# Performance work log

Hardware: AMD Instinct MI355X
Metric: run time of the kernel (lower is better)

Reference implementation:

```python
import jax, jax.numpy as jnp
import numpy as np

B, N, F, H = 2, 2048, 1024, 16
D = F // H  # head_dim = 64
SCALE = D ** -0.5


def setup_inputs() -> dict:
    key = jax.random.key(0)
    ks = jax.random.split(key, 5)
    std = F ** -0.5
    return {
        "x": jax.random.normal(ks[0], (B, N, F), dtype=jnp.float32),
        "Wq": jax.random.normal(ks[1], (F, F), dtype=jnp.float32) * std,
        "Wk": jax.random.normal(ks[2], (F, F), dtype=jnp.float32) * std,
        "Wv": jax.random.normal(ks[3], (F, F), dtype=jnp.float32) * std,
        "Wo": jax.random.normal(ks[4], (F, F), dtype=jnp.float32) * std,
        "bo": jnp.zeros((F,), dtype=jnp.float32),
    }


def reference(x, Wq, Wk, Wv, Wo, bo):
    b, n, f = x.shape
    # nn.Linear computes x @ W.T
    q = (x @ Wq.T).reshape(b, n, H, D).transpose(0, 2, 1, 3)  # bhnd
    k = (x @ Wk.T).reshape(b, n, H, D).transpose(0, 2, 1, 3)
    v = (x @ Wv.T).reshape(b, n, H, D).transpose(0, 2, 1, 3)
    score = jax.nn.softmax(jnp.einsum('bhif,bhjf->bhij', q, k) * SCALE, axis=-1)
    attn = jnp.einsum('bhij,bhjf->bihf', score, v)  # (b, n, h, d)
    o = attn.reshape(b, n, f) @ Wo.T + bo
    return o
```

## Files before the change

### kernel.cpp

```cpp
#include <hip/hip_runtime.h>
#include <hip/hip_bf16.h>

#define B_    2
#define NSEQ  2048
#define FDIM  1024
#define NH    16
#define HD    64
#define MTOT  (B_*NSEQ)
#define BHSZ  (NSEQ*HD)

typedef __bf16 bf16_t;
typedef __bf16 bf16x4 __attribute__((ext_vector_type(4)));
typedef __bf16 bf16x8 __attribute__((ext_vector_type(8)));
typedef float  f32x4  __attribute__((ext_vector_type(4)));

#define AS1 __attribute__((address_space(1)))
#define AS3 __attribute__((address_space(3)))

__device__ __forceinline__ void gld_lds16(const bf16_t* g, bf16_t* l) {
  __builtin_amdgcn_global_load_lds((const AS1 void*)g, (AS3 void*)l, 16, 0, 0);
}

__device__ __forceinline__ f32x4 mfma_pv(bf16x4 a, bf16x4 b, f32x4 c) {
#if defined(__HIP_DEVICE_COMPILE__)
#if __has_builtin(__builtin_amdgcn_mfma_f32_16x16x16bf16_1k)
  typedef short s4 __attribute__((ext_vector_type(4)));
  return __builtin_amdgcn_mfma_f32_16x16x16bf16_1k(
      __builtin_bit_cast(s4, a), __builtin_bit_cast(s4, b), c, 0, 0, 0);
#else
  asm("v_mfma_f32_16x16x16_bf16 %0, %1, %2, %0" : "+v"(c) : "v"(a), "v"(b));
  return c;
#endif
#else
  (void)a; (void)b;
  return c;
#endif
}

__device__ __forceinline__ float fexp2(float x) {
#if defined(__HIP_DEVICE_COMPILE__)
#if __has_builtin(__builtin_amdgcn_exp2f)
  return __builtin_amdgcn_exp2f(x);
#else
  return exp2f(x);
#endif
#else
  return exp2f(x);
#endif
}

extern "C" __global__ __launch_bounds__(256) void cast_all_k(
    const float* __restrict__ x,  const float* __restrict__ wq,
    const float* __restrict__ wk, const float* __restrict__ wv,
    const float* __restrict__ wo,
    bf16_t* __restrict__ xb,  bf16_t* __restrict__ wqb,
    bf16_t* __restrict__ wkb, bf16_t* __restrict__ wvb,
    bf16_t* __restrict__ wob)
{
  long t = (long)blockIdx.x * blockDim.x + threadIdx.x;
  long i = t * 4;
  const float* src; bf16_t* dst; long off;
  if      (i < 4194304L) { src = x;  dst = xb;  off = i; }
  else if (i < 5242880L) { src = wq; dst = wqb; off = i - 4194304L; }
  else if (i < 6291456L) { src = wk; dst = wkb; off = i - 5242880L; }
  else if (i < 7340032L) { src = wv; dst = wvb; off = i - 6291456L; }
  else                   { src = wo; dst = wob; off = i - 7340032L; }
  float4 v = *(const float4*)(src + off);
  bf16x4 o = { (bf16_t)v.x, (bf16_t)v.y, (bf16_t)v.z, (bf16_t)v.w };
  *(bf16x4*)(dst + off) = o;
}

extern "C" __global__ __launch_bounds__(256) void gemm_bt_k(
    const bf16_t* __restrict__ A,
    const bf16_t* __restrict__ Bq, const bf16_t* __restrict__ Bk,
    const bf16_t* __restrict__ Bv,
    bf16_t* __restrict__ oq, bf16_t* __restrict__ okk,
    bf16_t* __restrict__ ovt, float* __restrict__ oo,
    const float* __restrict__ bias, int mode_base)
{
  __shared__ __align__(16) bf16_t As[2*128*32];
  __shared__ __align__(16) bf16_t Bs[2*128*32];
  const int K = FDIM;
  int mode = mode_base + blockIdx.z;
  const bf16_t* Bw = (mode == 0) ? Bq : (mode == 1) ? Bk : (mode == 2) ? Bv : Bq;
  int m0 = blockIdx.y * 128, n0 = blockIdx.x * 128;
  int tid = threadIdx.x, lane = tid & 63, wave = tid >> 6;
  int g = lane >> 4, c = lane & 15;
  int wm = (wave >> 1) * 64, wn = (wave & 1) * 64;
  f32x4 acc[4][4];
  for (int i = 0; i < 4; ++i)
    for (int j = 0; j < 4; ++j)
      acc[i][j] = (f32x4){0.f, 0.f, 0.f, 0.f};

  int srow = lane >> 2;
  int scol = (lane & 3) * 8;

  for (int kt = 0; kt < K / 64; ++kt) {
    int kk = kt * 64;
    for (int cc = 0; cc < 2; ++cc) {
      int chunk = wave * 2 + cc;
      const bf16_t* ag = A  + (long)(m0 + chunk*16 + srow) * K + kk + scol;
      const bf16_t* bg = Bw + (long)(n0 + chunk*16 + srow) * K + kk + scol;
      gld_lds16(ag,      As + chunk * 512);
      gld_lds16(ag + 32, As + 4096 + chunk * 512);
      gld_lds16(bg,      Bs + chunk * 512);
      gld_lds16(bg + 32, Bs + 4096 + chunk * 512);
    }
    __syncthreads();
    bf16x8 af[4][2], bfr[4][2];
    for (int t = 0; t < 4; ++t) {
      af[t][0]  = *(const bf16x8*)(As + (wm + t*16 + c) * 32 + g * 8);
      af[t][1]  = *(const bf16x8*)(As + 4096 + (wm + t*16 + c) * 32 + g * 8);
      bfr[t][0] = *(const bf16x8*)(Bs + (wn + t*16 + c) * 32 + g * 8);
      bfr[t][1] = *(const bf16x8*)(Bs + 4096 + (wn + t*16 + c) * 32 + g * 8);
    }
    for (int mt = 0; mt < 4; ++mt)
      for (int nt = 0; nt < 4; ++nt) {
        acc[mt][nt] = __builtin_amdgcn_mfma_f32_16x16x32_bf16(
            af[mt][0], bfr[nt][0], acc[mt][nt], 0, 0, 0);
        acc[mt][nt] = __builtin_amdgcn_mfma_f32_16x16x32_bf16(
            af[mt][1], bfr[nt][1], acc[mt][nt], 0, 0, 0);
      }
    __syncthreads();
  }

  if (mode == 0) {
    const float QSC = 0.125f * 1.44269504088896340736f;
    for (int mt = 0; mt < 4; ++mt)
      for (int nt = 0; nt < 4; ++nt) {
        int n = n0 + wn + nt*16 + c;
        int h = n >> 6, d = n & 63;
        for (int r = 0; r < 4; ++r) {
          int m = m0 + wm + mt*16 + g*4 + r;
          int b = m >> 11, tok = m & 2047;
          oq[((long)(b*NH + h) * NSEQ + tok) * HD + d] =
              (bf16_t)(acc[mt][nt][r] * QSC);
        }
      }
  } else if (mode == 1) {
    for (int mt = 0; mt < 4; ++mt)
      for (int nt = 0; nt < 4; ++nt) {
        int n = n0 + wn + nt*16 + c;
        int h = n >> 6, d = n & 63;
        int kh = d >> 5, gK = (d >> 3) & 3, e = d & 7;
        for (int r = 0; r < 4; ++r) {
          int m = m0 + wm + mt*16 + g*4 + r;
          int b = m >> 11, tok = m & 2047;
          int tile = tok >> 6, mtA = (tok >> 4) & 3, cA = tok & 15;
          okk[(long)(b*NH + h) * BHSZ + tile*4096
              + (mtA*2 + kh)*512 + (gK*16 + cA)*8 + e] = (bf16_t)acc[mt][nt][r];
        }
      }
  } else if (mode == 2) {
    for (int mt = 0; mt < 4; ++mt)
      for (int nt = 0; nt < 4; ++nt) {
        int n = n0 + wn + nt*16 + c;
        int h = n >> 6, d = n & 63;
        int dtA = d >> 4, cA = d & 15;
        int m = m0 + wm + mt*16 + g*4;
        int b = m >> 11, tok = m & 2047;
        int tile = tok >> 6, mtA = (tok >> 4) & 3, gA = (tok >> 2) & 3;
        bf16x4 pk = { (bf16_t)acc[mt][nt][0], (bf16_t)acc[mt][nt][1],
                      (bf16_t)acc[mt][nt][2], (bf16_t)acc[mt][nt][3] };
        *(bf16x4*)(ovt + (long)(b*NH + h) * BHSZ + tile*4096
                   + (mtA*4 + dtA)*256 + (cA*4 + gA)*4) = pk;
      }
  } else {
    for (int mt = 0; mt < 4; ++mt)
      for (int nt = 0; nt < 4; ++nt) {
        int n = n0 + wn + nt*16 + c;
        float bv = bias[n];
        for (int r = 0; r < 4; ++r) {
          int m = m0 + wm + mt*16 + g*4 + r;
          oo[(long)m * FDIM + n] = acc[mt][nt][r] + bv;
        }
      }
  }
}

extern "C" __global__ __launch_bounds__(512) void attn_fused_k(
    const bf16_t* __restrict__ q, const bf16_t* __restrict__ k,
    const bf16_t* __restrict__ vt, bf16_t* __restrict__ attn)
{
  __shared__ __align__(16) char arena[65536];
  __shared__ float Ll[128];
  int bh = blockIdx.y;
  int tid = threadIdx.x, lane = tid & 63, wave = tid >> 6;
  int g = lane >> 4, c = lane & 15;
  int qg = wave & 3, half = wave >> 2;
  int qw = blockIdx.x * 128 + qg * 32;
  const bf16_t* Q  = q  + (long)bh * NSEQ * HD;
  const bf16_t* Kf = k  + (long)bh * BHSZ;
  const bf16_t* Vf = vt + (long)bh * BHSZ;

  bf16x8 bQ[2][2];
#pragma unroll
  for (int s = 0; s < 2; ++s)
#pragma unroll
    for (int hh = 0; hh < 2; ++hh)
      bQ[s][hh] = *(const bf16x8*)(Q + (long)(qw + s*16 + c) * HD + hh*32 + g*8);

  f32x4 acc[2][4];
  f32x4 lsum[2];
#pragma unroll
  for (int s = 0; s < 2; ++s) {
#pragma unroll
    for (int dt = 0; dt < 4; ++dt) acc[s][dt] = (f32x4){0.f, 0.f, 0.f, 0.f};
    lsum[s] = (f32x4){0.f, 0.f, 0.f, 0.f};
  }

  int w4 = wave & 3, ln = lane;
  const int NT = NSEQ / 128;
  int kbase = half * (NSEQ / 2);

  auto stage = [&](int buf, int k0) {
    bf16_t* Kb = (bf16_t*)(arena + buf * 32768 + half * 16384);
    bf16_t* Vb = Kb + 4096;
    long tbase = (long)(k0 >> 6) * 4096;
#pragma unroll
    for (int j = 0; j < 2; ++j) {
      int ch = j*4 + w4;
      gld_lds16(Kf + tbase + ch*512 + ln*8, Kb + ch*512);
      gld_lds16(Vf + tbase + ch*512 + ln*8, Vb + ch*512);
    }
  };

  stage(0, kbase);
  __syncthreads();

  for (int kt = 0; kt < NT; ++kt) {
    int cur = kt & 1;
    if (kt + 1 < NT) stage(cur ^ 1, kbase + (kt + 1) * 64);

    const bf16_t* Kb = (const bf16_t*)(arena + cur * 32768 + half * 16384);
    const bf16_t* Vb = Kb + 4096;

    f32x4 St[2][4];
#pragma unroll
    for (int mt = 0; mt < 4; ++mt) {
      bf16x8 k0f = *(const bf16x8*)(Kb + (mt*2 + 0) * 512 + lane * 8);
      bf16x8 k1f = *(const bf16x8*)(Kb + (mt*2 + 1) * 512 + lane * 8);
#pragma unroll
      for (int s = 0; s < 2; ++s) {
        f32x4 z = (f32x4){0.f, 0.f, 0.f, 0.f};
        z = __builtin_amdgcn_mfma_f32_16x16x32_bf16(k0f, bQ[s][0], z, 0, 0, 0);
        z = __builtin_amdgcn_mfma_f32_16x16x32_bf16(k1f, bQ[s][1], z, 0, 0, 0);
        St[s][mt] = z;
      }
    }

    bf16x4 bP[2][4];
#pragma unroll
    for (int s = 0; s < 2; ++s)
#pragma unroll
      for (int mt = 0; mt < 4; ++mt) {
#pragma unroll
        for (int r = 0; r < 4; ++r) {
          float p = fexp2(St[s][mt][r]);
          St[s][mt][r] = p;
          lsum[s][r] += p;
        }
        bP[s][mt] = (bf16x4){(bf16_t)St[s][mt][0], (bf16_t)St[s][mt][1],
                             (bf16_t)St[s][mt][2], (bf16_t)St[s][mt][3]};
      }

#pragma unroll
    for (int mt = 0; mt < 4; ++mt)
#pragma unroll
      for (int dt = 0; dt < 4; ++dt) {
        bf16x4 aV = *(const bf16x4*)(Vb + (mt*4 + dt) * 256 + (c*4 + g) * 4);
        acc[0][dt] = mfma_pv(aV, bP[0][mt], acc[0][dt]);
        acc[1][dt] = mfma_pv(aV, bP[1][mt], acc[1][dt]);
      }

    __syncthreads();
  }

  float lp[2];
#pragma unroll
  for (int s = 0; s < 2; ++s) {
    float p = (lsum[s][0] + lsum[s][1]) + (lsum[s][2] + lsum[s][3]);
    p += __shfl_xor(p, 16);
    p += __shfl_xor(p, 32);
    lp[s] = p;
  }

  float* Opart = (float*)arena;
  bf16_t* Tb = (bf16_t*)(arena + 36864);
  if (half == 1) {
#pragma unroll
    for (int s = 0; s < 2; ++s) {
      int qrow = qg*32 + s*16 + c;
#pragma unroll
      for (int dt = 0; dt < 4; ++dt)
        *(f32x4*)(Opart + qrow*72 + dt*16 + g*4) = acc[s][dt];
      if (g == 0) Ll[qrow] = lp[s];
    }
  }
  __syncthreads();
  if (half == 0) {
#pragma unroll
    for (int s = 0; s < 2; ++s) {
      int qrow = qg*32 + s*16 + c;
      float inv = 1.f / (lp[s] + Ll[qrow]);
#pragma unroll
      for (int dt = 0; dt < 4; ++dt) {
        f32x4 part = *(const f32x4*)(Opart + qrow*72 + dt*16 + g*4);
#pragma unroll
        for (int r = 0; r < 4; ++r)
          Tb[qrow*80 + dt*16 + g*4 + r] =
              (bf16_t)((acc[s][dt][r] + part[r]) * inv);
      }
    }
  }
  __syncthreads();
  int b = bh >> 4, h = bh & 15;
  int row = tid >> 2, dseg = (tid & 3) * 16;
  const bf16_t* src = Tb + row*80 + dseg;
  bf16_t* dst = attn + ((long)(b * NSEQ + blockIdx.x*128 + row)) * FDIM + h * HD + dseg;
  *(bf16x8*)(dst)     = *(const bf16x8*)(src);
  *(bf16x8*)(dst + 8) = *(const bf16x8*)(src + 8);
}

extern "C" void kernel_launch(void* const* d_in, const int* in_sizes, int n_in,
                              void* d_out, int out_size, void* d_ws, size_t ws_size,
                              hipStream_t stream)
{
  const float* x  = (const float*)d_in[0];
  const float* wq = (const float*)d_in[1];
  const float* wk = (const float*)d_in[2];
  const float* wv = (const float*)d_in[3];
  const float* wo = (const float*)d_in[4];
  const float* bo = (const float*)d_in[5];
  float* out = (float*)d_out;
  char* ws = (char*)d_ws;

  const size_t MB = 1024 * 1024;
  bf16_t* xb    = (bf16_t*)(ws);
  bf16_t* wqb   = (bf16_t*)(ws + 8  * MB);
  bf16_t* wkb   = (bf16_t*)(ws + 10 * MB);
  bf16_t* wvb   = (bf16_t*)(ws + 12 * MB);
  bf16_t* wob   = (bf16_t*)(ws + 14 * MB);
  bf16_t* q_ws  = (bf16_t*)(ws + 16 * MB);
  bf16_t* k_ws  = (bf16_t*)(ws + 24 * MB);
  bf16_t* vt_ws = (bf16_t*)(ws + 32 * MB);
  bf16_t* at_ws = (bf16_t*)(ws + 40 * MB);

  hipLaunchKernelGGL(cast_all_k, dim3(8192), dim3(256), 0, stream,
                     x, wq, wk, wv, wo, xb, wqb, wkb, wvb, wob);

  hipLaunchKernelGGL(gemm_bt_k, dim3(8, 32, 3), dim3(256), 0, stream,
                     xb, wqb, wkb, wvb, q_ws, k_ws, vt_ws,
                     (float*)nullptr, (const float*)nullptr, 0);

  hipLaunchKernelGGL(attn_fused_k, dim3(16, 32), dim3(512), 0, stream,
                     q_ws, k_ws, vt_ws, at_ws);

  hipLaunchKernelGGL(gemm_bt_k, dim3(8, 32, 1), dim3(256), 0, stream,
                     at_ws, wob, wob, wob,
                     (bf16_t*)nullptr, (bf16_t*)nullptr, (bf16_t*)nullptr,
                     out, bo, 3);
}
```

Measured before the change: 203.9 us.

## Stage QKV GEMM epilogue through LDS for coalesced 16-byte stores; use natural exp

The Q/K/V projection epilogue now writes the accumulator tile into a padded LDS buffer, then re-reads it and emits 16-byte vector global stores in the attention-friendly layouts, replacing scattered 2-byte stores. The Q scale drops the log2(e) factor, and the attention kernel switches from exp2 to __expf to match. This targets uncoalesced write traffic in the GEMM epilogue, at the cost of extra LDS use, a barrier and more index arithmetic. __expf may lower to a multiply plus exp2, adding one multiply per score element.

```diff
diff --git a/kernel.cpp b/kernel.cpp
--- a/kernel.cpp
+++ b/kernel.cpp
@@ -34,18 +34,6 @@
 #else
   (void)a; (void)b;
   return c;
-#endif
-}
-
-__device__ __forceinline__ float fexp2(float x) {
-#if defined(__HIP_DEVICE_COMPILE__)
-#if __has_builtin(__builtin_amdgcn_exp2f)
-  return __builtin_amdgcn_exp2f(x);
-#else
-  return exp2f(x);
-#endif
-#else
-  return exp2f(x);
 #endif
 }
 
@@ -78,8 +66,9 @@
     bf16_t* __restrict__ ovt, float* __restrict__ oo,
     const float* __restrict__ bias, int mode_base)
 {
-  __shared__ __align__(16) bf16_t As[2*128*32];
-  __shared__ __align__(16) bf16_t Bs[2*128*32];
+  __shared__ __align__(16) char garena[33792];
+  bf16_t* As = (bf16_t*)garena;
+  bf16_t* Bs = (bf16_t*)(garena + 16384);
   const int K = FDIM;
   int mode = mode_base + blockIdx.z;
   const bf16_t* Bw = (mode == 0) ? Bq : (mode == 1) ? Bk : (mode == 2) ? Bv : Bq;
@@ -124,48 +113,7 @@
     __syncthreads();
   }
 
-  if (mode == 0) {
-    const float QSC = 0.125f * 1.44269504088896340736f;
-    for (int mt = 0; mt < 4; ++mt)
-      for (int nt = 0; nt < 4; ++nt) {
-        int n = n0 + wn + nt*16 + c;
-        int h = n >> 6, d = n & 63;
-        for (int r = 0; r < 4; ++r) {
-          int m = m0 + wm + mt*16 + g*4 + r;
-          int b = m >> 11, tok = m & 2047;
-          oq[((long)(b*NH + h) * NSEQ + tok) * HD + d] =
-              (bf16_t)(acc[mt][nt][r] * QSC);
-        }
-      }
-  } else if (mode == 1) {
-    for (int mt = 0; mt < 4; ++mt)
-      for (int nt = 0; nt < 4; ++nt) {
-        int n = n0 + wn + nt*16 + c;
-        int h = n >> 6, d = n & 63;
-        int kh = d >> 5, gK = (d >> 3) & 3, e = d & 7;
-        for (int r = 0; r < 4; ++r) {
-          int m = m0 + wm + mt*16 + g*4 + r;
-          int b = m >> 11, tok = m & 2047;
-          int tile = tok >> 6, mtA = (tok >> 4) & 3, cA = tok & 15;
-          okk[(long)(b*NH + h) * BHSZ + tile*4096
-              + (mtA*2 + kh)*512 + (gK*16 + cA)*8 + e] = (bf16_t)acc[mt][nt][r];
-        }
-      }
-  } else if (mode == 2) {
-    for (int mt = 0; mt < 4; ++mt)
-      for (int nt = 0; nt < 4; ++nt) {
-        int n = n0 + wn + nt*16 + c;
-        int h = n >> 6, d = n & 63;
-        int dtA = d >> 4, cA = d & 15;
-        int m = m0 + wm + mt*16 + g*4;
-        int b = m >> 11, tok = m & 2047;
-        int tile = tok >> 6, mtA = (tok >> 4) & 3, gA = (tok >> 2) & 3;
-        bf16x4 pk = { (bf16_t)acc[mt][nt][0], (bf16_t)acc[mt][nt][1],
-                      (bf16_t)acc[mt][nt][2], (bf16_t)acc[mt][nt][3] };
-        *(bf16x4*)(ovt + (long)(b*NH + h) * BHSZ + tile*4096
-                   + (mtA*4 + dtA)*256 + (cA*4 + gA)*4) = pk;
-      }
-  } else {
+  if (mode == 3) {
     for (int mt = 0; mt < 4; ++mt)
       for (int nt = 0; nt < 4; ++nt) {
         int n = n0 + wn + nt*16 + c;
@@ -175,6 +123,72 @@
           oo[(long)m * FDIM + n] = acc[mt][nt][r] + bv;
         }
       }
+    return;
+  }
+
+  bf16_t* Tl = (bf16_t*)garena;
+  float sc = (mode == 0) ? 0.125f : 1.0f;
+  if (mode < 2) {
+    for (int mt = 0; mt < 4; ++mt)
+      for (int nt = 0; nt < 4; ++nt) {
+        int nloc = wn + nt*16 + c;
+        for (int r = 0; r < 4; ++r) {
+          int mloc = wm + mt*16 + g*4 + r;
+          Tl[mloc*132 + nloc] = (bf16_t)(acc[mt][nt][r] * sc);
+        }
+      }
+  } else {
+    for (int mt = 0; mt < 4; ++mt)
+      for (int nt = 0; nt < 4; ++nt) {
+        int nloc = wn + nt*16 + c;
+        int mloc = wm + mt*16 + g*4;
+        bf16x4 pk = { (bf16_t)acc[mt][nt][0], (bf16_t)acc[mt][nt][1],
+                      (bf16_t)acc[mt][nt][2], (bf16_t)acc[mt][nt][3] };
+        *(bf16x4*)(Tl + nloc*132 + mloc) = pk;
+      }
+  }
+  __syncthreads();
+
+  int b = m0 >> 11, m0loc = m0 & 2047;
+  int h0 = n0 >> 6, tile0 = m0loc >> 6;
+#pragma unroll
+  for (int u = 0; u < 8; ++u) {
+    int chunk = u * 256 + tid;
+    bf16_t* dst;
+    int sidx;
+    if (mode == 0) {
+      int headloc = chunk >> 10, o = chunk & 1023;
+      int tokloc = o >> 3, dd = (o & 7) * 8;
+      sidx = tokloc*132 + headloc*64 + dd;
+      dst = oq + ((long)(b*NH + h0 + headloc) * NSEQ + m0loc) * HD + (long)o * 8;
+    } else if (mode == 1) {
+      int region = chunk >> 9, o = chunk & 511;
+      int headloc = region >> 1, t = region & 1;
+      int f = o >> 6, rest = o & 63;
+      int mtA = f >> 1, kh = f & 1, gK = rest >> 4, cA = rest & 15;
+      int tokloc = t*64 + mtA*16 + cA;
+      sidx = tokloc*132 + headloc*64 + kh*32 + gK*8;
+      dst = okk + (long)(b*NH + h0 + headloc) * BHSZ
+            + (long)(tile0 + t) * 4096 + (long)o * 8;
+    } else {
+      int region = chunk >> 9, o = chunk & 511;
+      int headloc = region >> 1, t = region & 1;
+      int frag = o >> 5, so = o & 31;
+      int mtA = frag >> 2, dtA = frag & 3;
+      int slot0 = so * 2;
+      int cA = slot0 >> 2, gA0 = slot0 & 3;
+      int k0loc = t*64 + mtA*16 + gA0*4;
+      int nloc = headloc*64 + dtA*16 + cA;
+      sidx = nloc*132 + k0loc;
+      dst = ovt + (long)(b*NH + h0 + headloc) * BHSZ
+            + (long)(tile0 + t) * 4096 + (long)o * 8;
+    }
+    bf16x4 lo = *(const bf16x4*)(Tl + sidx);
+    bf16x4 hi = *(const bf16x4*)(Tl + sidx + 4);
+    bf16x8 v;
+#pragma unroll
+    for (int i = 0; i < 4; ++i) { v[i] = lo[i]; v[i+4] = hi[i]; }
+    *(bf16x8*)dst = v;
   }
 }
 
@@ -256,7 +270,7 @@
       for (int mt = 0; mt < 4; ++mt) {
 #pragma unroll
         for (int r = 0; r < 4; ++r) {
-          float p = fexp2(St[s][mt][r]);
+          float p = __expf(St[s][mt][r]);
           St[s][mt][r] = p;
           lsum[s][r] += p;
         }
```

New measurement: 199.6 us. 1.02x faster.
